# Performance work log

Hardware: AMD Instinct MI355X
Metric: run time of the kernel (lower is better)

The kernel has to match this reference:

```python
import jax, jax.numpy as jnp
import numpy as np
from jax import lax

NUM_QUBITS = 4
NUM_LAYERS = 2
EPS = 1e-5  # BatchNorm eps; eval mode with running_mean=0, running_var=1


def _cnot_ring_matrix():
    # CNOT(0,1); CNOT(1,2); CNOT(2,3); CNOT(3,0) as one 16x16 permutation.
    # PennyLane convention: wire 0 is the most-significant bit of the basis index.
    M = np.zeros((16, 16), dtype=np.complex64)
    for b in range(16):
        bb = b
        for cw, tw in [(0, 1), (1, 2), (2, 3), (3, 0)]:
            if (bb >> (3 - cw)) & 1:
                bb ^= 1 << (3 - tw)
        M[bb, b] = 1.0
    return M

CNOT_RING = jnp.asarray(_cnot_ring_matrix())
# ZSIGNS[w, b] = <b|Z_w|b> = +/-1
ZSIGNS = jnp.asarray(np.array([[1.0 - 2.0 * ((b >> (3 - w)) & 1) for b in range(16)]
                               for w in range(NUM_QUBITS)], dtype=np.float32))


def conv_bn_relu(x, w, b, gamma, beta):
    # Conv2d(k=3, pad=1) + BatchNorm2d (eval: mean=0, var=1) + ReLU, NCHW
    x = lax.conv_general_dilated(x, w, (1, 1), ((1, 1), (1, 1)),
                                 dimension_numbers=('NCHW', 'OIHW', 'NCHW'))
    x = x + b[None, :, None, None]
    x = gamma[None, :, None, None] * x * (1.0 / np.sqrt(1.0 + EPS)) + beta[None, :, None, None]
    return jax.nn.relu(x)


def maxpool2(x):
    return lax.reduce_window(x, -jnp.inf, lax.max, (1, 1, 2, 2), (1, 1, 2, 2), 'VALID')


def avgpool2(x):
    return lax.reduce_window(x, 0.0, lax.add, (1, 1, 2, 2), (1, 1, 2, 2), 'VALID') * 0.25


def quantum_layer(x, weights):
    # x: [B, 16] softmax outputs. Amplitude-encode (abs + L2 normalize), then
    # BasicEntanglerLayers (RX rotations + CNOT ring) x NUM_LAYERS, then <Z_i>.
    psi = jnp.abs(x)
    psi = psi / jnp.linalg.norm(psi, axis=1, keepdims=True)
    psi = psi.astype(jnp.complex64)  # [B, 16] batched statevectors
    for l in range(NUM_LAYERS):
        c = jnp.cos(weights[l] * 0.5).astype(jnp.complex64)
        s = jnp.sin(weights[l] * 0.5).astype(jnp.complex64)
        U = jnp.ones((1, 1), dtype=jnp.complex64)
        for q in range(NUM_QUBITS):
            g = jnp.stack([jnp.stack([c[q], -1j * s[q]]),
                           jnp.stack([-1j * s[q], c[q]])])  # RX(theta_q)
            U = jnp.kron(U, g)
        U = CNOT_RING @ U  # rotations first, then entangling ring
        psi = psi @ U.T    # batched apply: [B,16] x [16,16]
    probs = jnp.real(psi * jnp.conj(psi))  # [B, 16]
    return probs @ ZSIGNS.T                # [B, 4] Pauli-Z expvals


def setup_inputs() -> dict:
    key = jax.random.key(0)
    ks = jax.random.split(key, 16)
    B = 1024
    f32 = jnp.float32

    def w(k, shape, fan_in):
        return jax.random.normal(k, shape, dtype=f32) * np.float32(1.0 / np.sqrt(fan_in))

    inp = {
        'x': jax.random.normal(ks[0], (B, 3, 32, 32), dtype=f32),
        'conv1_w': w(ks[1], (32, 3, 3, 3), 3 * 9), 'conv1_b': jnp.zeros((32,), f32),
        'bn1_g': jnp.ones((32,), f32), 'bn1_b': jnp.zeros((32,), f32),
        'conv2_w': w(ks[2], (64, 32, 3, 3), 32 * 9), 'conv2_b': jnp.zeros((64,), f32),
        'bn2_g': jnp.ones((64,), f32), 'bn2_b': jnp.zeros((64,), f32),
        'conv3_w': w(ks[3], (128, 64, 3, 3), 64 * 9), 'conv3_b': jnp.zeros((128,), f32),
        'bn3_g': jnp.ones((128,), f32), 'bn3_b': jnp.zeros((128,), f32),
        'fr1_w': w(ks[4], (512, 2048), 2048), 'fr1_b': jnp.zeros((512,), f32),
        'fr2_w': w(ks[5], (16, 512), 512), 'fr2_b': jnp.zeros((16,), f32),
        'q_weights': jax.random.uniform(ks[6], (NUM_LAYERS, NUM_QUBITS), dtype=f32,
                                        minval=0.0, maxval=2.0 * np.pi),
        'h1_w': w(ks[7], (128, 4), 4), 'h1_b': jnp.zeros((128,), f32),
        'bnh_g': jnp.ones((128,), f32), 'bnh_b': jnp.zeros((128,), f32),
        'h2_w': w(ks[8], (100, 128), 128), 'h2_b': jnp.zeros((100,), f32),
    }
    return inp


def reference(x, conv1_w, conv1_b, bn1_g, bn1_b, conv2_w, conv2_b, bn2_g, bn2_b,
              conv3_w, conv3_b, bn3_g, bn3_b, fr1_w, fr1_b, fr2_w, fr2_b,
              q_weights, h1_w, h1_b, bnh_g, bnh_b, h2_w, h2_b):
    # classical_net (CIFAR100 branch)
    h = conv_bn_relu(x, conv1_w, conv1_b, bn1_g, bn1_b)
    h = maxpool2(h)                                   # [B,32,16,16]
    h = conv_bn_relu(h, conv2_w, conv2_b, bn2_g, bn2_b)
    h = maxpool2(h)                                   # [B,64,8,8]
    h = conv_bn_relu(h, conv3_w, conv3_b, bn3_g, bn3_b)  # [B,128,8,8]
    h = avgpool2(h)                                   # AdaptiveAvgPool2d((4,4)): 8->4
    h = h.reshape(h.shape[0], -1)                     # [B, 2048]
    # feature_reducer
    h = jax.nn.relu(h @ fr1_w.T + fr1_b)
    f = jax.nn.softmax(h @ fr2_w.T + fr2_b, axis=1)   # [B, 16]
    # quantum layer (batched 4-qubit statevector sim)
    q = quantum_layer(f, q_weights)                   # [B, 4]
    # head (BN eval-mode, Dropout inactive)
    y = q @ h1_w.T + h1_b
    y = bnh_g * y * (1.0 / np.sqrt(1.0 + EPS)) + bnh_b
    y = jax.nn.relu(y)
    return y @ h2_w.T + h2_b                          # [B, 100]
```

## Files before the change

### kernel.cpp

```cpp
#include <hip/hip_runtime.h>
#include <math.h>

#define NB 1024
static constexpr float BN_INV = 0.99999500003749975f;

typedef __attribute__((ext_vector_type(8))) short short8;
typedef __attribute__((ext_vector_type(4))) short s16x4;
typedef __attribute__((ext_vector_type(4))) float f32x4;

__device__ inline short f2bf(float f) {
  union { float f; unsigned u; } v;
  v.f = f;
  unsigned u = v.u;
  u += 0x7fff + ((u >> 16) & 1);
  return (short)(u >> 16);
}

__global__ void k_prepack(const float* __restrict__ c1w, const float* __restrict__ c1b,
                          const float* __restrict__ g1, const float* __restrict__ be1,
                          const float* __restrict__ c2w, const float* __restrict__ c2b,
                          const float* __restrict__ g2, const float* __restrict__ be2,
                          const float* __restrict__ c3w, const float* __restrict__ c3b,
                          const float* __restrict__ g3, const float* __restrict__ be3,
                          const float* __restrict__ fr2w, const float* __restrict__ h2w,
                          short* __restrict__ wp1, short* __restrict__ wp2,
                          short* __restrict__ wp3, float* __restrict__ scsh,
                          float* __restrict__ w2t, float* __restrict__ h2wt) {
  int i = blockIdx.x * 256 + threadIdx.x;
  int stride = gridDim.x * 256;
  for (int e = i; e < 2048; e += stride) {
    int j = e & 7, lane = (e >> 3) & 63, ct = (e >> 9) & 1, mf = e >> 10;
    int co = ct * 16 + (lane & 15), k = (lane >> 4) * 8 + j;
    int kx = (k >> 2) & 3, c = k & 3;
    float v = 0.f;
    if (mf == 0) {
      int ky = k >> 4;
      if (kx < 3 && c < 3) v = c1w[(co * 3 + c) * 9 + ky * 3 + kx] * g1[co] * BN_INV;
    } else {
      if (k < 16 && kx < 3 && c < 3)
        v = c1w[(co * 3 + c) * 9 + 6 + kx] * g1[co] * BN_INV;
    }
    wp1[e] = f2bf(v);
  }
  for (int e = i; e < 18432; e += stride) {
    int j = e & 7, lane = (e >> 3) & 63, ct = (e >> 9) & 3, off = e >> 11;
    int co = ct * 16 + (lane & 15), ci = (lane >> 4) * 8 + j;
    wp2[e] = f2bf(c2w[(co * 32 + ci) * 9 + off]);
  }
  for (int e = i; e < 73728; e += stride) {
    int j = e & 7, lane = (e >> 3) & 63, ct = (e >> 9) & 7, oh = e >> 12;
    int half = oh & 1, off = oh >> 1;
    int co = ct * 16 + (lane & 15), ci = half * 32 + (lane >> 4) * 8 + j;
    wp3[e] = f2bf(c3w[(co * 64 + ci) * 9 + off]);
  }
  for (int e = i; e < 8192; e += stride) {
    int k = e >> 4, j = e & 15;
    w2t[k * 20 + j] = fr2w[j * 512 + k];
  }
  for (int e = i; e < 12800; e += stride) {
    int j = e / 100, k = e - j * 100;
    h2wt[j * 104 + k] = h2w[k * 128 + j];
  }
  if (i < 64) {
    float sc = g2[i] * BN_INV;
    scsh[i] = sc;
    scsh[64 + i] = sc * c2b[i] + be2[i];
  } else if (i < 192) {
    int c = i - 64;
    float sc = g3[c] * BN_INV;
    scsh[128 + c] = sc;
    scsh[256 + c] = sc * c3b[c] + be3[c];
  } else if (i < 224) {
    int c = i - 192;
    scsh[384 + c] = g1[c] * BN_INV * c1b[c] + be1[c];
  }
}

__global__ __launch_bounds__(512) void k_convfused(
    const float* __restrict__ x, const short* __restrict__ wp1,
    const short* __restrict__ wp2, const short* __restrict__ wp3,
    const float* __restrict__ scsh, const float* __restrict__ fr1w,
    short* __restrict__ wfr1, short* __restrict__ out3 ) {
  __shared__ __align__(16) char smem[49600];
  const int tid = threadIdx.x;
  const int bx = blockIdx.x;

  if (bx < 128) {
    int i = bx * 512 + tid;
    for (int e = i; e < 524288; e += 128 * 512) {
      float2 f = ((const float2*)fr1w)[e];
      unsigned lo = (unsigned)(unsigned short)f2bf(f.x);
      unsigned hi = (unsigned)(unsigned short)f2bf(f.y);
      ((unsigned*)wfr1)[e] = (hi << 16) | lo;
    }
    return;
  }

  short* inT = (short*)smem;
  short* tile1 = (short*)(smem + 25920);
  short* inT3 = (short*)(smem + 35200);

  const int b = bx - 128;
  const int wid = tid >> 6, lane = tid & 63, q = lane >> 4, n = lane & 15;

  const float* xb = x + b * 3072;
  f32x4 xf0 = ((const f32x4*)xb)[tid];
  f32x4 xf1;
  if (tid < 256) xf1 = ((const f32x4*)xb)[tid + 512];
  for (int i = tid; i < 1088; i += 512) {
    int cidx = i >> 4, w = i & 15, r, cc;
    if (cidx < 18) { r = 0; cc = cidx; }
    else if (cidx < 36) { r = 17; cc = cidx - 18; }
    else { int j = cidx - 36; r = 1 + (j >> 1); cc = (j & 1) * 17; }
    ((int*)&inT[(r * 18 + cc) * 40])[w] = 0;
  }
  for (int i = tid; i < 264; i += 512) {
    int cidx = i >> 1, w = i & 1, r, cc;
    if (cidx < 34) { r = 0; cc = cidx; }
    else if (cidx < 68) { r = 33; cc = cidx - 34; }
    else { int j = cidx - 68; r = 1 + (j >> 1); cc = (j & 1) * 33; }
    ((int*)&tile1[(r * 34 + cc) * 4])[w] = 0;
  }
  if (tid < 8) ((int*)tile1)[2312 + tid] = 0;
  for (int i = tid; i < 1152; i += 512) {
    int cidx = i >> 5, w = i & 31, r, cc;
    if (cidx < 10) { r = 0; cc = cidx; }
    else if (cidx < 20) { r = 9; cc = cidx - 10; }
    else { int j = cidx - 20; r = 1 + (j >> 1); cc = (j & 1) * 9; }
    ((int*)&inT3[(r * 10 + cc) * 72])[w] = 0;
  }
  {
    int e0 = tid * 4;
#pragma unroll
    for (int jj = 0; jj < 4; ++jj) {
      int e = e0 + jj;
      int c = e >> 10, rem = e & 1023, iy = rem >> 5, ix = rem & 31;
      tile1[((iy + 1) * 34 + (ix + 1)) * 4 + c] = f2bf(xf0[jj]);
    }
    if (tid < 256) {
      int e1 = (tid + 512) * 4;
#pragma unroll
      for (int jj = 0; jj < 4; ++jj) {
        int e = e1 + jj;
        int c = e >> 10, rem = e & 1023, iy = rem >> 5, ix = rem & 31;
        tile1[((iy + 1) * 34 + (ix + 1)) * 4 + c] = f2bf(xf1[jj]);
      }
    }
  }
  __syncthreads();

  {
    const short8* wv1 = (const short8*)wp1;
    short8 a00 = wv1[0 * 64 + lane];
    short8 a01 = wv1[1 * 64 + lane];
    short8 a10 = wv1[2 * 64 + lane];
    short8 a11 = wv1[3 * 64 + lane];
    const int ky0 = q >> 1, kx0 = (q & 1) * 2;
    float sh1[2][4];
#pragma unroll
    for (int ct = 0; ct < 2; ++ct)
#pragma unroll
      for (int r = 0; r < 4; ++r) sh1[ct][r] = scsh[384 + ct * 16 + q * 4 + r];

#pragma unroll
    for (int h = 0; h < 2; ++h) {
      const int xb0 = h * 16 + n;
      f32x4 acc[2][4];
#pragma unroll
      for (int ct = 0; ct < 2; ++ct)
#pragma unroll
        for (int yy = 0; yy < 4; ++yy) acc[ct][yy] = (f32x4)0.f;
#pragma unroll
      for (int yy = 0; yy < 4; ++yy) {
        int y = 4 * wid + yy;
        const short* p0 = &tile1[((y + ky0) * 34 + xb0 + kx0) * 4];
        const short* p1 = &tile1[((y + 2) * 34 + xb0 + kx0) * 4];
        s16x4 b0l = *(const s16x4*)p0, b0h = *(const s16x4*)(p0 + 4);
        s16x4 b1l = *(const s16x4*)p1, b1h = *(const s16x4*)(p1 + 4);
        short8 B0 = __builtin_shufflevector(b0l, b0h, 0, 1, 2, 3, 4, 5, 6, 7);
        short8 B1 = __builtin_shufflevector(b1l, b1h, 0, 1, 2, 3, 4, 5, 6, 7);
        acc[0][yy] = __builtin_amdgcn_mfma_f32_16x16x32_bf16(a00, B0, acc[0][yy], 0, 0, 0);
        acc[0][yy] = __builtin_amdgcn_mfma_f32_16x16x32_bf16(a10, B1, acc[0][yy], 0, 0, 0);
        acc[1][yy] = __builtin_amdgcn_mfma_f32_16x16x32_bf16(a01, B0, acc[1][yy], 0, 0, 0);
        acc[1][yy] = __builtin_amdgcn_mfma_f32_16x16x32_bf16(a11, B1, acc[1][yy], 0, 0, 0);
      }
#pragma unroll
      for (int ct = 0; ct < 2; ++ct)
#pragma unroll
        for (int yp = 0; yp < 2; ++yp)
#pragma unroll
          for (int r = 0; r < 4; ++r) {
            float v0 = fmaxf(acc[ct][2 * yp][r] + sh1[ct][r], 0.f);
            float v1 = fmaxf(acc[ct][2 * yp + 1][r] + sh1[ct][r], 0.f);
            float m = fmaxf(v0, v1);
            m = fmaxf(m, __shfl_xor(m, 1));
            if ((n & 1) == 0) {
              int co = ct * 16 + q * 4 + r;
              int yq = 2 * wid + yp, xq = 8 * h + (n >> 1);
              inT[((yq + 1) * 18 + (xq + 1)) * 40 + co] = f2bf(m);
            }
          }
    }
  }
  __syncthreads();

  {
    const short8* wv = (const short8*)wp2;
    f32x4 acc[2][4];
#pragma unroll
    for (int t = 0; t < 2; ++t)
#pragma unroll
      for (int ct = 0; ct < 4; ++ct) acc[t][ct] = (f32x4)0.f;

#pragma unroll
    for (int off = 0; off < 9; ++off) {
      const int ky = off / 3, kx = off % 3;
      short8 a[4];
#pragma unroll
      for (int ct = 0; ct < 4; ++ct) a[ct] = wv[(off * 4 + ct) * 64 + lane];
#pragma unroll
      for (int t = 0; t < 2; ++t) {
        int y = 2 * wid + t;
        short8 bf = *(const short8*)&inT[((y + ky) * 18 + (n + kx)) * 40 + q * 8];
#pragma unroll
        for (int ct = 0; ct < 4; ++ct)
          acc[t][ct] = __builtin_amdgcn_mfma_f32_16x16x32_bf16(a[ct], bf,
                                                               acc[t][ct], 0, 0, 0);
      }
    }

    const float* sc2 = scsh;
    const float* sh2 = scsh + 64;
#pragma unroll
    for (int ct = 0; ct < 4; ++ct)
#pragma unroll
      for (int r = 0; r < 4; ++r) {
        int co = ct * 16 + q * 4 + r;
        float v0 = fmaf(sc2[co], acc[0][ct][r], sh2[co]);
        float v1 = fmaf(sc2[co], acc[1][ct][r], sh2[co]);
        v0 = fmaxf(v0, 0.f);
        v1 = fmaxf(v1, 0.f);
        float m0 = fmaxf(v0, __shfl_xor(v0, 1));
        float m1 = fmaxf(v1, __shfl_xor(v1, 1));
        float m = fmaxf(m0, m1);
        if ((n & 1) == 0)
          inT3[((wid + 1) * 10 + (n >> 1) + 1) * 72 + co] = f2bf(m);
      }
  }
  __syncthreads();

  {
    const short8* wv = (const short8*)wp3;
    f32x4 acc[2][2];
#pragma unroll
    for (int c = 0; c < 2; ++c)
#pragma unroll
      for (int tt = 0; tt < 2; ++tt) acc[c][tt] = (f32x4)0.f;

    const int ct0 = (wid >> 1) * 2;
    const int t0 = (wid & 1) * 2;
#pragma unroll
    for (int off = 0; off < 9; ++off) {
      const int ky = off / 3, kx = off % 3;
#pragma unroll
      for (int half = 0; half < 2; ++half) {
        short8 a[2];
#pragma unroll
        for (int c = 0; c < 2; ++c)
          a[c] = wv[((off * 2 + half) * 8 + ct0 + c) * 64 + lane];
#pragma unroll
        for (int tt = 0; tt < 2; ++tt) {
          int y = 2 * (t0 + tt) + (n >> 3), xx = n & 7;
          short8 bf = *(const short8*)&inT3[((y + ky) * 10 + (xx + kx)) * 72 +
                                            half * 32 + q * 8];
#pragma unroll
          for (int c = 0; c < 2; ++c)
            acc[c][tt] = __builtin_amdgcn_mfma_f32_16x16x32_bf16(a[c], bf,
                                                                 acc[c][tt], 0, 0, 0);
        }
      }
    }

    const float* sc3 = scsh + 128;
    const float* sh3 = scsh + 256;
#pragma unroll
    for (int c = 0; c < 2; ++c) {
      int ct = ct0 + c;
#pragma unroll
      for (int tt = 0; tt < 2; ++tt) {
        int t = t0 + tt;
#pragma unroll
        for (int r = 0; r < 4; ++r) {
          int co = ct * 16 + q * 4 + r;
          float v = fmaf(sc3[co], acc[c][tt][r], sh3[co]);
          v = fmaxf(v, 0.f);
          float s = v + __shfl_xor(v, 1);
          s += __shfl_xor(s, 8);
          if ((n & 9) == 0)
            out3[(size_t)b * 2048 + co * 16 + t * 4 + (n >> 1)] = f2bf(s * 0.25f);
        }
      }
    }
  }
}

__global__ __launch_bounds__(256) void k_fr1m(
    const short* __restrict__ A, const short* __restrict__ W,
    const float* __restrict__ bias, float* __restrict__ C) {
  __shared__ __align__(16) short As[2 * 2304];
  __shared__ __align__(16) short Bs[2 * 2304];
  const int m0 = blockIdx.x * 32;
  const int n0 = blockIdx.y * 32;
  const int tid = threadIdx.x;
  const int w = tid >> 6, lane = tid & 63, q = lane >> 4, n = lane & 15;
  const int mt = w >> 1, nt = w & 1;
  const int srow = tid >> 3, sc = tid & 7;

  f32x4 acc = (f32x4)0.f;
  const short* Ab = A + (size_t)(m0 + srow) * 2048 + sc * 8;
  const short* Wb = W + (size_t)(n0 + srow) * 2048 + sc * 8;

  short8 av = *(const short8*)Ab;
  short8 bv = *(const short8*)Wb;
  for (int it = 0; it < 32; ++it) {
    short* Asb = As + (it & 1) * 2304;
    short* Bsb = Bs + (it & 1) * 2304;
    *(short8*)&Asb[srow * 72 + sc * 8] = av;
    *(short8*)&Bsb[srow * 72 + sc * 8] = bv;
    if (it < 31) {
      av = *(const short8*)(Ab + (it + 1) * 64);
      bv = *(const short8*)(Wb + (it + 1) * 64);
    }
    __syncthreads();
#pragma unroll
    for (int kk = 0; kk < 2; ++kk) {
      short8 bfrag = *(const short8*)&Bsb[(nt * 16 + n) * 72 + kk * 32 + q * 8];
      short8 afrag = *(const short8*)&Asb[(mt * 16 + n) * 72 + kk * 32 + q * 8];
      acc = __builtin_amdgcn_mfma_f32_16x16x32_bf16(afrag, bfrag, acc, 0, 0, 0);
    }
  }
#pragma unroll
  for (int r = 0; r < 4; ++r) {
    int m = m0 + mt * 16 + q * 4 + r;
    int nn = n0 + nt * 16 + n;
    C[(size_t)m * 512 + nn] = fmaxf(acc[r] + bias[nn], 0.f);
  }
}

__global__ __launch_bounds__(64) void k_tail(
    const float* __restrict__ H, const float* __restrict__ w2t,
    const float* __restrict__ b2, const float* __restrict__ qw,
    const float* __restrict__ h1w, const float* __restrict__ h1b,
    const float* __restrict__ bg, const float* __restrict__ bb,
    const float* __restrict__ h2wt, const float* __restrict__ h2b,
    float* __restrict__ out) {
  __shared__ float hbuf[512];
  __shared__ float ybuf[128];
  const int b = blockIdx.x;
  const int lane = threadIdx.x;
  const float* hrow = H + b * 512;
  *(float4*)&hbuf[lane * 4] = *(const float4*)&hrow[lane * 4];
  *(float4*)&hbuf[256 + lane * 4] = *(const float4*)&hrow[256 + lane * 4];
  __syncthreads();

  const int j = lane & 15;
  const int grpk = lane >> 4;
  float partial = 0.f;
  {
    const float* wcol = w2t + j;
    const int kbase = grpk * 128;
#pragma unroll 8
    for (int k = 0; k < 128; ++k)
      partial = fmaf(wcol[(kbase + k) * 20], hbuf[kbase + k], partial);
  }
  partial += __shfl_xor(partial, 16);
  partial += __shfl_xor(partial, 32);
  float logit = partial + b2[j];

  float m = logit;
#pragma unroll
  for (int d = 1; d < 16; d <<= 1) m = fmaxf(m, __shfl_xor(m, d));
  float e = expf(logit - m);
  float s = e;
#pragma unroll
  for (int d = 1; d < 16; d <<= 1) s += __shfl_xor(s, d);
  float p = e / s;

  float n2 = p * p;
#pragma unroll
  for (int d = 1; d < 16; d <<= 1) n2 += __shfl_xor(n2, d);
  float amp = p / sqrtf(n2);
  float re = amp, im = 0.f;

#pragma unroll
  for (int l = 0; l < 2; ++l) {
#pragma unroll
    for (int q = 0; q < 4; ++q) {
      float th = qw[l * 4 + q] * 0.5f;
      float c = cosf(th), sn = sinf(th);
      int mask = 1 << (3 - q);
      float pre = __shfl_xor(re, mask);
      float pim = __shfl_xor(im, mask);
      float nre = fmaf(c, re, sn * pim);
      float nim = fmaf(c, im, -sn * pre);
      re = nre;
      im = nim;
    }
    int src = j;
    if (src & 1) src ^= 8;
    if (src & 2) src ^= 1;
    if (src & 4) src ^= 2;
    if (src & 8) src ^= 4;
    int srclane = (lane & 48) | src;
    re = __shfl(re, srclane);
    im = __shfl(im, srclane);
  }

  float prob = re * re + im * im;
  float qv[4];
#pragma unroll
  for (int w = 0; w < 4; ++w) {
    float sgn = ((j >> (3 - w)) & 1) ? -1.f : 1.f;
    float cwv = prob * sgn;
    cwv += __shfl_xor(cwv, 1);
    cwv += __shfl_xor(cwv, 2);
    cwv += __shfl_xor(cwv, 4);
    cwv += __shfl_xor(cwv, 8);
    qv[w] = cwv;
  }

#pragma unroll
  for (int t = 0; t < 2; ++t) {
    int jj = lane + 64 * t;
    float4 hw = *(const float4*)&h1w[jj * 4];
    float y = h1b[jj];
    y = fmaf(hw.x, qv[0], y);
    y = fmaf(hw.y, qv[1], y);
    y = fmaf(hw.z, qv[2], y);
    y = fmaf(hw.w, qv[3], y);
    y = fmaf(bg[jj] * BN_INV, y, bb[jj]);
    ybuf[jj] = fmaxf(y, 0.f);
  }
  __syncthreads();

#pragma unroll
  for (int t = 0; t < 2; ++t) {
    int k = lane + 64 * t;
    if (k < 100) {
      const float* wc = h2wt + k;
      float o = h2b[k];
#pragma unroll 8
      for (int jj = 0; jj < 128; ++jj)
        o = fmaf(wc[jj * 104], ybuf[jj], o);
      out[b * 100 + k] = o;
    }
  }
}

extern "C" void kernel_launch(void* const* d_in, const int* in_sizes, int n_in,
                              void* d_out, int out_size, void* d_ws,
                              size_t ws_size, hipStream_t stream) {
  const float* x = (const float*)d_in[0];
  const float* c1w = (const float*)d_in[1];
  const float* c1b = (const float*)d_in[2];
  const float* g1 = (const float*)d_in[3];
  const float* be1 = (const float*)d_in[4];
  const float* c2w = (const float*)d_in[5];
  const float* c2b = (const float*)d_in[6];
  const float* g2 = (const float*)d_in[7];
  const float* be2 = (const float*)d_in[8];
  const float* c3w = (const float*)d_in[9];
  const float* c3b = (const float*)d_in[10];
  const float* g3 = (const float*)d_in[11];
  const float* be3 = (const float*)d_in[12];
  const float* fr1w = (const float*)d_in[13];
  const float* fr1b = (const float*)d_in[14];
  const float* fr2w = (const float*)d_in[15];
  const float* fr2b = (const float*)d_in[16];
  const float* qwts = (const float*)d_in[17];
  const float* h1w = (const float*)d_in[18];
  const float* h1b = (const float*)d_in[19];
  const float* bhg = (const float*)d_in[20];
  const float* bhb = (const float*)d_in[21];
  const float* h2w = (const float*)d_in[22];
  const float* h2b = (const float*)d_in[23];
  float* out = (float*)d_out;

  float* ws = (float*)d_ws;
  short* out3bf = (short*)ws;
  float* h1 = ws + 1048576;
  short* wfr1 = (short*)(ws + 1572864);
  short* wp2 = (short*)(ws + 2097152);
  short* wp3 = (short*)(ws + 2106368);
  float* scsh = ws + 2143232;
  short* wp1 = (short*)(ws + 2143744);
  float* w2t = ws + 2144768;
  float* h2wt = ws + 2155008;

  k_prepack<<<96, 256, 0, stream>>>(c1w, c1b, g1, be1, c2w, c2b, g2, be2, c3w,
                                    c3b, g3, be3, fr2w, h2w, wp1, wp2, wp3,
                                    scsh, w2t, h2wt);
  k_convfused<<<NB + 128, 512, 0, stream>>>(x, wp1, wp2, wp3, scsh, fr1w, wfr1,
                                            out3bf);
  k_fr1m<<<dim3(32, 16), 256, 0, stream>>>(out3bf, wfr1, fr1b, h1);
  k_tail<<<NB, 64, 0, stream>>>(h1, w2t, fr2b, qwts, h1w, h1b, bhg, bhb, h2wt,
                                h2b, out);
}
```

Measured before the change: 175.3 us.

## Repartition conv2/conv3 MFMA work per wave to keep weights register-resident

Conv2 and conv3 work is re-split across the 8 waves. Each wave now owns one 16-channel output tile and several spatial rows, where before each wave covered several channel tiles for fewer rows. Because of this, each wave's weight fragments for all 9 taps are loaded once into registers, and that load is issued before the barrier so it overlaps the wait. This cuts repeated global weight fetches per MFMA but raises register pressure (18 short8 fragments for conv3 and 8 f32x4 accumulators for conv2), which could lower occupancy.

Result: slower. 185.3 us (+5.7%).

```diff
diff --git a/kernel.cpp b/kernel.cpp
--- a/kernel.cpp
+++ b/kernel.cpp
@@ -202,81 +202,79 @@
           }
     }
   }
+
+  const int cg = wid & 3, rg = wid >> 2;
+  short8 a2[9];
+  {
+    const short8* wv = (const short8*)wp2;
+#pragma unroll
+    for (int off = 0; off < 9; ++off) a2[off] = wv[(off * 4 + cg) * 64 + lane];
+  }
   __syncthreads();
 
   {
-    const short8* wv = (const short8*)wp2;
-    f32x4 acc[2][4];
-#pragma unroll
-    for (int t = 0; t < 2; ++t)
-#pragma unroll
-      for (int ct = 0; ct < 4; ++ct) acc[t][ct] = (f32x4)0.f;
+    f32x4 acc[8];
+#pragma unroll
+    for (int t = 0; t < 8; ++t) acc[t] = (f32x4)0.f;
 
 #pragma unroll
     for (int off = 0; off < 9; ++off) {
       const int ky = off / 3, kx = off % 3;
-      short8 a[4];
-#pragma unroll
-      for (int ct = 0; ct < 4; ++ct) a[ct] = wv[(off * 4 + ct) * 64 + lane];
-#pragma unroll
-      for (int t = 0; t < 2; ++t) {
-        int y = 2 * wid + t;
+#pragma unroll
+      for (int t = 0; t < 8; ++t) {
+        int y = rg * 8 + t;
         short8 bf = *(const short8*)&inT[((y + ky) * 18 + (n + kx)) * 40 + q * 8];
-#pragma unroll
-        for (int ct = 0; ct < 4; ++ct)
-          acc[t][ct] = __builtin_amdgcn_mfma_f32_16x16x32_bf16(a[ct], bf,
-                                                               acc[t][ct], 0, 0, 0);
+        acc[t] = __builtin_amdgcn_mfma_f32_16x16x32_bf16(a2[off], bf, acc[t], 0, 0, 0);
       }
     }
 
     const float* sc2 = scsh;
     const float* sh2 = scsh + 64;
 #pragma unroll
-    for (int ct = 0; ct < 4; ++ct)
+    for (int p = 0; p < 4; ++p)
 #pragma unroll
       for (int r = 0; r < 4; ++r) {
-        int co = ct * 16 + q * 4 + r;
-        float v0 = fmaf(sc2[co], acc[0][ct][r], sh2[co]);
-        float v1 = fmaf(sc2[co], acc[1][ct][r], sh2[co]);
+        int co = cg * 16 + q * 4 + r;
+        float v0 = fmaf(sc2[co], acc[2 * p][r], sh2[co]);
+        float v1 = fmaf(sc2[co], acc[2 * p + 1][r], sh2[co]);
         v0 = fmaxf(v0, 0.f);
         v1 = fmaxf(v1, 0.f);
         float m0 = fmaxf(v0, __shfl_xor(v0, 1));
         float m1 = fmaxf(v1, __shfl_xor(v1, 1));
         float m = fmaxf(m0, m1);
         if ((n & 1) == 0)
-          inT3[((wid + 1) * 10 + (n >> 1) + 1) * 72 + co] = f2bf(m);
+          inT3[((rg * 4 + p + 1) * 10 + (n >> 1) + 1) * 72 + co] = f2bf(m);
       }
   }
+
+  short8 a3[2][9];
+  {
+    const short8* wv = (const short8*)wp3;
+#pragma unroll
+    for (int off = 0; off < 9; ++off)
+#pragma unroll
+      for (int half = 0; half < 2; ++half)
+        a3[half][off] = wv[((off * 2 + half) * 8 + wid) * 64 + lane];
+  }
   __syncthreads();
 
   {
-    const short8* wv = (const short8*)wp3;
-    f32x4 acc[2][2];
-#pragma unroll
-    for (int c = 0; c < 2; ++c)
-#pragma unroll
-      for (int tt = 0; tt < 2; ++tt) acc[c][tt] = (f32x4)0.f;
-
-    const int ct0 = (wid >> 1) * 2;
-    const int t0 = (wid & 1) * 2;
+    f32x4 acc[4];
+#pragma unroll
+    for (int tt = 0; tt < 4; ++tt) acc[tt] = (f32x4)0.f;
+
 #pragma unroll
     for (int off = 0; off < 9; ++off) {
       const int ky = off / 3, kx = off % 3;
 #pragma unroll
       for (int half = 0; half < 2; ++half) {
-        short8 a[2];
-#pragma unroll
-        for (int c = 0; c < 2; ++c)
-          a[c] = wv[((off * 2 + half) * 8 + ct0 + c) * 64 + lane];
-#pragma unroll
-        for (int tt = 0; tt < 2; ++tt) {
-          int y = 2 * (t0 + tt) + (n >> 3), xx = n & 7;
+#pragma unroll
+        for (int tt = 0; tt < 4; ++tt) {
+          int y = 2 * tt + (n >> 3), xx = n & 7;
           short8 bf = *(const short8*)&inT3[((y + ky) * 10 + (xx + kx)) * 72 +
                                             half * 32 + q * 8];
-#pragma unroll
-          for (int c = 0; c < 2; ++c)
-            acc[c][tt] = __builtin_amdgcn_mfma_f32_16x16x32_bf16(a[c], bf,
-                                                                 acc[c][tt], 0, 0, 0);
+          acc[tt] = __builtin_amdgcn_mfma_f32_16x16x32_bf16(a3[half][off], bf,
+                                                            acc[tt], 0, 0, 0);
         }
       }
     }
@@ -284,23 +282,17 @@
     const float* sc3 = scsh + 128;
     const float* sh3 = scsh + 256;
 #pragma unroll
-    for (int c = 0; c < 2; ++c) {
-      int ct = ct0 + c;
-#pragma unroll
-      for (int tt = 0; tt < 2; ++tt) {
-        int t = t0 + tt;
-#pragma unroll
-        for (int r = 0; r < 4; ++r) {
-          int co = ct * 16 + q * 4 + r;
-          float v = fmaf(sc3[co], acc[c][tt][r], sh3[co]);
-          v = fmaxf(v, 0.f);
-          float s = v + __shfl_xor(v, 1);
-          s += __shfl_xor(s, 8);
-          if ((n & 9) == 0)
-            out3[(size_t)b * 2048 + co * 16 + t * 4 + (n >> 1)] = f2bf(s * 0.25f);
-        }
+    for (int tt = 0; tt < 4; ++tt)
+#pragma unroll
+      for (int r = 0; r < 4; ++r) {
+        int co = wid * 16 + q * 4 + r;
+        float v = fmaf(sc3[co], acc[tt][r], sh3[co]);
+        v = fmaxf(v, 0.f);
+        float s = v + __shfl_xor(v, 1);
+        s += __shfl_xor(s, 8);
+        if ((n & 9) == 0)
+          out3[(size_t)b * 2048 + co * 16 + tt * 4 + (n >> 1)] = f2bf(s * 0.25f);
       }
-    }
   }
 }
 
```
